# Optimization experiments

Measured on AMD Instinct MI355X. Metric: run time of the kernel, lower is better.

Reference implementation:

```python
import jax, jax.numpy as jnp
import numpy as np

GAMMA = 0.9
SCALE_BASE = 512.0


def _xpos(x, downscale=False):
    """XPOS rotary embedding (torchscale variant) applied to x: (B, L, D)."""
    B, L, D = x.shape
    half = D // 2
    # per-channel magnitude base: ((2i) + 0.4*D) / (1.4*D), i over even channels
    scale_vec = (jnp.arange(0, D, 2, dtype=jnp.float32) + 0.4 * D) / (1.4 * D)  # (half,)
    power = jnp.arange(L, dtype=jnp.float32) / SCALE_BASE                        # (L,)
    scale = scale_vec[None, :] ** power[:, None]                                 # (L, half)
    if downscale:
        scale = 1.0 / scale
    # fixed sinusoidal frequencies over `half` dims
    inv_freq = 1.0 / (10000.0 ** (jnp.arange(half, dtype=jnp.float32) / half))   # (half,)
    sinusoid = jnp.arange(L, dtype=jnp.float32)[:, None] * inv_freq[None, :]     # (L, half)
    sin = jnp.repeat(jnp.sin(sinusoid) * scale, 2, axis=-1)                      # (L, D) interleaved dup
    cos = jnp.repeat(jnp.cos(sinusoid) * scale, 2, axis=-1)
    # rotate_every_two: (x0,x1,x2,x3,...) -> (-x1,x0,-x3,x2,...)
    x_even = x[..., 0::2]
    x_odd = x[..., 1::2]
    rot = jnp.stack((-x_odd, x_even), axis=-1).reshape(x.shape)
    return x * cos + rot * sin


def _get_D(seq_len):
    n = jnp.arange(seq_len, dtype=jnp.float32)[:, None]
    m = jnp.arange(seq_len, dtype=jnp.float32)[None, :]
    D = GAMMA ** jnp.abs(n - m)  # non-causal decay, no NaNs since gamma > 0
    return D


def setup_inputs() -> dict:
    key = jax.random.key(0)
    k1, k2, k3, k4 = jax.random.split(key, 4)
    B, L, H, Dh = 8, 2048, 1024, 1024
    X = jax.random.normal(k1, (B, L, H), dtype=jnp.float32)
    W_Q = jax.random.normal(k2, (H, Dh), dtype=jnp.float32) / H
    W_K = jax.random.normal(k3, (H, Dh), dtype=jnp.float32) / H
    W_V = jax.random.normal(k4, (H, Dh), dtype=jnp.float32) / H
    return {"X": X, "W_Q": W_Q, "W_K": W_K, "W_V": W_V}


def reference(X, W_Q, W_K, W_V):
    B, L, H = X.shape
    D = _get_D(L)                       # (L, L)
    Q = _xpos(X @ W_Q)                  # (B, L, Dh)
    K = _xpos(X @ W_K, downscale=True)  # (B, L, Dh)
    V = X @ W_V                         # (B, L, Dv)
    scores = jnp.einsum('bqd,bkd->bqk', Q, K)   # (B, L, L)
    p_attn = jax.nn.softmax(scores, axis=-1)
    p_attn = p_attn * D[None, :, :]              # elementwise decay AFTER softmax
    return jnp.einsum('bqk,bkv->bqv', p_attn, V)
```

## Files before the change

kernel.cpp:

```cpp
#include <hip/hip_runtime.h>
#include <math.h>


#define LDIM 2048
#define HDIM 1024
#define MTOT 16384

typedef unsigned short u16;
typedef unsigned int u32;
typedef __attribute__((ext_vector_type(4))) float f32x4;
typedef __attribute__((ext_vector_type(8))) short s16x8;

#define GLD16(gp, lp) __builtin_amdgcn_global_load_lds( \
    (const __attribute__((address_space(1))) void*)(gp), \
    (__attribute__((address_space(3))) void*)(lp), 16, 0, 0)

__device__ __forceinline__ u16 f2bf(float f) {
    unsigned u = __float_as_uint(f);
    return (u16)((u + 0x7FFFu + ((u >> 16) & 1u)) >> 16);
}

__device__ __forceinline__ void sincos_rev(float ang, float* sn, float* cs) {
    double dr = (double)ang * 0.15915494309189535;
    dr -= __builtin_floor(dr);
    float fr = (float)dr;
    float s_, c_;
    asm("v_sin_f32 %0, %1" : "=v"(s_) : "v"(fr));
    asm("v_cos_f32 %0, %1" : "=v"(c_) : "v"(fr));
    *sn = s_; *cs = c_;
}

__device__ __forceinline__ void gemm256q(const u16* __restrict__ A,
                                         const u16* __restrict__ B,
                                         int lda, int ldb, int K, int m0, int n0,
                                         char* smem, int tid, f32x4 (*acc)[4])
{
    const int wv = tid >> 6, ln = tid & 63;
    const int wm = wv >> 2, wn = wv & 3;
    const int lr = ln & 15, lg = ln >> 4;
    const int srow = tid >> 3;
    const int scol = ((tid & 7) ^ (srow & 7)) * 8;

    const u16* ap[4];
    const u16* bp[4];
#pragma unroll
    for (int r = 0; r < 4; ++r) {
        ap[r] = A + (size_t)(m0 + r * 64 + srow) * lda + scol;
        bp[r] = B + (size_t)(n0 + r * 64 + srow) * ldb + scol;
    }

    int arow[8], brow[4];
#pragma unroll
    for (int fm = 0; fm < 8; ++fm) arow[fm] = (wm * 128 + fm * 16 + lr) * 128;
#pragma unroll
    for (int fn = 0; fn < 4; ++fn) brow[fn] = 32768 + (wn * 64 + fn * 16 + lr) * 128;
    int slotb[2];
#pragma unroll
    for (int kk = 0; kk < 2; ++kk) slotb[kk] = (((kk << 2) | lg) ^ (lr & 7)) << 4;

#define SGA0(e_) do{ char* d_=smem+(e_)*65536+tid*16;       GLD16(ap[0],d_); GLD16(ap[1],d_+8192); ap[0]+=64; ap[1]+=64; }while(0)
#define SGA1(e_) do{ char* d_=smem+(e_)*65536+16384+tid*16; GLD16(ap[2],d_); GLD16(ap[3],d_+8192); ap[2]+=64; ap[3]+=64; }while(0)
#define SGB0(e_) do{ char* d_=smem+(e_)*65536+32768+tid*16; GLD16(bp[0],d_); GLD16(bp[1],d_+8192); bp[0]+=64; bp[1]+=64; }while(0)
#define SGB1(e_) do{ char* d_=smem+(e_)*65536+49152+tid*16; GLD16(bp[2],d_); GLD16(bp[3],d_+8192); bp[2]+=64; bp[3]+=64; }while(0)

#define RD_A(Bb_, mh) do {                                                    \
        _Pragma("unroll") for (int fm_ = 0; fm_ < 4; ++fm_)                   \
            _Pragma("unroll") for (int kk_ = 0; kk_ < 2; ++kk_)               \
                aq[fm_ * 2 + kk_] = *(const s16x8*)((Bb_) +                   \
                    arow[(mh) * 4 + fm_] + slotb[kk_]);                       \
    } while (0)
#define RD_B(Bb_, nh, dst) do {                                               \
        _Pragma("unroll") for (int fn_ = 0; fn_ < 2; ++fn_)                   \
            _Pragma("unroll") for (int kk_ = 0; kk_ < 2; ++kk_)               \
                dst[fn_ * 2 + kk_] = *(const s16x8*)((Bb_) +                  \
                    brow[(nh) * 2 + fn_] + slotb[kk_]);                       \
    } while (0)

#define MFMA16(mh, nh, bq_) do { __builtin_amdgcn_s_setprio(1);               \
        _Pragma("unroll") for (int fm_ = 0; fm_ < 4; ++fm_)                   \
            _Pragma("unroll") for (int fn_ = 0; fn_ < 2; ++fn_)               \
                _Pragma("unroll") for (int kk_ = 0; kk_ < 2; ++kk_)           \
                    acc[(mh) * 4 + fm_][(nh) * 2 + fn_] =                     \
                        __builtin_amdgcn_mfma_f32_16x16x32_bf16(              \
                            aq[fm_ * 2 + kk_], bq_[fn_ * 2 + kk_],            \
                            acc[(mh) * 4 + fm_][(nh) * 2 + fn_], 0, 0, 0);    \
        __builtin_amdgcn_s_setprio(0); } while (0)

#define BAR do { __builtin_amdgcn_sched_barrier(0);                           \
                 __builtin_amdgcn_s_barrier();                                \
                 __builtin_amdgcn_sched_barrier(0); } while (0)

    const int nk = K >> 6;

    SGA0(0); SGB0(0); SGA1(0); SGB1(0);

    s16x8 aq[8], b0[4], b1[4];

#pragma unroll 1
    for (int t = 0; t < nk; ++t) {
        const int d = t & 1, e = d ^ 1;
        const bool pre = (t + 1 < nk);
        const char* Bb = smem + d * 65536;

        if (pre) { SGA0(e); SGB0(e);
                   asm volatile("s_waitcnt vmcnt(4)" ::: "memory"); }
        else     { asm volatile("s_waitcnt vmcnt(0)" ::: "memory"); }
        BAR;
        RD_A(Bb, 0); RD_B(Bb, 0, b0); if (pre) SGA1(e);
        BAR; MFMA16(0, 0, b0); BAR;
        RD_B(Bb, 1, b1); if (pre) SGB1(e);
        BAR; MFMA16(0, 1, b1); BAR;
        RD_A(Bb, 1);
        BAR; MFMA16(1, 1, b1); BAR;
        BAR; MFMA16(1, 0, b0); BAR;
    }
    __syncthreads();
#undef SGA0
#undef SGA1
#undef SGB0
#undef SGB1
#undef RD_A
#undef RD_B
#undef MFMA16
#undef BAR
}

__global__ __launch_bounds__(256) void prep_all(
    const float* __restrict__ X,
    const float* __restrict__ Wq, const float* __restrict__ Wk,
    const float* __restrict__ Wv,
    u16* __restrict__ Xb, u16* __restrict__ WT,
    u32* __restrict__ CSq, u32* __restrict__ CSk)
{
    __shared__ float L[64][65];
    const int bid = blockIdx.x;
    if (bid < 2048) {
        const int n4 = MTOT * HDIM / 4;
        int i = bid * 256 + threadIdx.x;
        const int stride = 2048 * 256;
        for (; i < n4; i += stride) {
            float4 v = ((const float4*)X)[i];
            ushort4 o = make_ushort4(f2bf(v.x), f2bf(v.y), f2bf(v.z), f2bf(v.w));
            ((ushort4*)Xb)[i] = o;
        }
    } else if (bid < 4096) {
        const int l = bid - 2048;
        for (int ih = threadIdx.x; ih < 512; ih += 256) {
            float invf = exp2f(-13.287712379549449f * (1.f / 512.f) * (float)ih);
            float sn, cs;
            sincos_rev((float)l * invf, &sn, &cs);
            float l2sv = log2f(((float)(2 * ih) + 409.6f) * (1.f / 1433.6f));
            float e = (float)l * (1.f / 512.f) * l2sv;
            float sq = exp2f(e), sk = exp2f(-e);
            CSq[l * 512 + ih] = (u32)f2bf(cs * sq) | ((u32)f2bf(sn * sq) << 16);
            CSk[l * 512 + ih] = (u32)f2bf(cs * sk) | ((u32)f2bf(sn * sk) << 16);
        }
    } else {
        const int r = bid - 4096;
        const int z = r >> 8;
        const int y = (r >> 4) & 15;
        const int x = r & 15;
        const float* Wz = (z == 0) ? Wq : (z == 1) ? Wk : Wv;
        u16* Oz = WT + (size_t)z * HDIM * HDIM;
        const int k0 = y * 64, n0 = x * 64;
        const int t = threadIdx.x;
        const int r_ = t >> 4, c4 = (t & 15) * 4;
#pragma unroll
        for (int it = 0; it < 4; ++it) {
            const int row = it * 16 + r_;
            float4 v = *(const float4*)&Wz[(size_t)(k0 + row) * HDIM + n0 + c4];
            L[row][c4 + 0] = v.x; L[row][c4 + 1] = v.y;
            L[row][c4 + 2] = v.z; L[row][c4 + 3] = v.w;
        }
        __syncthreads();
#pragma unroll
        for (int it = 0; it < 4; ++it) {
            const int orow = it * 16 + r_;
            ushort4 o = make_ushort4(f2bf(L[c4 + 0][orow]), f2bf(L[c4 + 1][orow]),
                                     f2bf(L[c4 + 2][orow]), f2bf(L[c4 + 3][orow]));
            *(ushort4*)&Oz[(size_t)(n0 + orow) * HDIM + k0 + c4] = o;
        }
    }
}

__global__ __launch_bounds__(512, 2) void qkv_gemm(
    const u16* __restrict__ Xb, const u16* __restrict__ WT,
    const u32* __restrict__ CSq, const u32* __restrict__ CSk,
    u16* __restrict__ Qb, u16* __restrict__ Kb, u16* __restrict__ Vt)
{
    __shared__ __align__(16) char smem[256 * 264 * 2];
    const int bid = blockIdx.x;
    const int xcd = bid & 7, t = bid >> 3;
    const int m8 = t & 7;
    const int n_ = (t >> 3) & 3;
    const int z  = t >> 5;
    const int m0 = (xcd * 8 + m8) * 256;
    const int n0 = n_ * 256;
    const int tid = threadIdx.x;

    f32x4 acc[8][4] = {};

    gemm256q(Xb, WT + (size_t)z * HDIM * HDIM, HDIM, HDIM, HDIM, m0, n0, smem, tid, acc);

    const int wv = tid >> 6, ln = tid & 63;
    const int wm = wv >> 2, wn = wv & 3;
    const int lr = ln & 15, lg = ln >> 4;
    const int l0 = m0 & (LDIM - 1);
    u16* T = (u16*)smem;

    if (z < 2) {
        const u32* CS = (z == 0) ? CSq : CSk;
#pragma unroll
        for (int fn = 0; fn < 4; ++fn) {
            const int gc = n0 + wn * 64 + fn * 16 + lr;
            const int ih = gc >> 1;
            const float sgn = (gc & 1) ? 1.f : -1.f;
            const u32* tb = CS + (size_t)l0 * 512 + ih;
#pragma unroll
            for (int fm = 0; fm < 8; ++fm) {
#pragma unroll
                for (int reg = 0; reg < 4; ++reg) {
                    const int rowl = wm * 128 + fm * 16 + lg * 4 + reg;
                    u32 v = tb[(size_t)rowl * 512];
                    float cs = __uint_as_float(v << 16);
                    float sn = __uint_as_float(v & 0xFFFF0000u);
                    float c = acc[fm][fn][reg];
                    float p = __shfl_xor(c, 1);
                    T[rowl * 264 + wn * 64 + fn * 16 + lr] =
                        f2bf(c * cs + sgn * p * sn);
                }
            }
        }
        __syncthreads();
        u16* Out = (z == 0) ? Qb : Kb;
        const int row_ = tid >> 5, slot = tid & 31;
#pragma unroll
        for (int g = 0; g < 16; ++g) {
            const int row = g * 16 + row_;
            s16x8 v = *(const s16x8*)&T[row * 264 + slot * 8];
            *(s16x8*)&Out[(size_t)(m0 + row) * HDIM + n0 + slot * 8] = v;
        }
    } else {
#pragma unroll
        for (int fn = 0; fn < 4; ++fn)
#pragma unroll
            for (int fm = 0; fm < 8; ++fm) {
                ushort4 o = make_ushort4(f2bf(acc[fm][fn][0]), f2bf(acc[fm][fn][1]),
                                         f2bf(acc[fm][fn][2]), f2bf(acc[fm][fn][3]));
                *(ushort4*)&T[(wn * 64 + fn * 16 + lr) * 264 +
                              wm * 128 + fm * 16 + lg * 4] = o;
            }
        __syncthreads();
        const int b = m0 >> 11;
        const int row_ = tid >> 5, slot = tid & 31;
#pragma unroll
        for (int g = 0; g < 16; ++g) {
            const int row = g * 16 + row_;
            s16x8 v = *(const s16x8*)&T[row * 264 + slot * 8];
            *(s16x8*)&Vt[((size_t)b * HDIM + n0 + row) * LDIM + l0 + slot * 8] = v;
        }
    }
}

__global__ __launch_bounds__(512, 2) void qk_gemm(
    const u16* __restrict__ Q, const u16* __restrict__ Km,
    u16* __restrict__ Wm, float* __restrict__ Zp)
{
    __shared__ __align__(16) char smem[256 * 264 * 2];
    __shared__ float Zl[4][256];
    const int bid = blockIdx.x;
    const int b = bid & 7, t = bid >> 3;
    const int mt = t & 7;
    const int nt = t >> 3;
    const int m0 = mt * 256;
    const int n0 = nt * 256;
    const int tid = threadIdx.x;

    f32x4 acc[8][4] = {};

    gemm256q(Q + (size_t)b * LDIM * HDIM, Km + (size_t)b * LDIM * HDIM,
             HDIM, HDIM, HDIM, m0, n0, smem, tid, acc);

    const int wv = tid >> 6, ln = tid & 63;
    const int wm = wv >> 2, wn = wv & 3;
    const int lr = ln & 15, lg = ln >> 4;
    u16* T = (u16*)smem;
    const float LOG2E = 1.4426950408889634f;
    const float LOG2G = -0.15200309344504997f;

#pragma unroll
    for (int fm = 0; fm < 8; ++fm) {
        float ps[4] = {0.f, 0.f, 0.f, 0.f};
#pragma unroll
        for (int fn = 0; fn < 4; ++fn) {
            const int gk = n0 + wn * 64 + fn * 16 + lr;
#pragma unroll
            for (int reg = 0; reg < 4; ++reg) {
                const int mloc = wm * 128 + fm * 16 + lg * 4 + reg;
                const int gq = m0 + mloc;
                float t1 = acc[fm][fn][reg] * LOG2E;
                float e = exp2f(t1);
                int dd = gq - gk; dd = dd < 0 ? -dd : dd;
                ps[reg] += e;
                T[mloc * 264 + wn * 64 + fn * 16 + lr] =
                    f2bf(exp2f(t1 + (float)dd * LOG2G));
            }
        }
#pragma unroll
        for (int reg = 0; reg < 4; ++reg) {
            float s = ps[reg];
            s += __shfl_xor(s, 1); s += __shfl_xor(s, 2);
            s += __shfl_xor(s, 4); s += __shfl_xor(s, 8);
            if (lr == 0)
                Zl[wn][wm * 128 + fm * 16 + lg * 4 + reg] = s;
        }
    }
    __syncthreads();

    const int row_ = tid >> 5, slot = tid & 31;
#pragma unroll
    for (int g = 0; g < 16; ++g) {
        const int row = g * 16 + row_;
        s16x8 v = *(const s16x8*)&T[row * 264 + slot * 8];
        *(s16x8*)&Wm[((size_t)b * LDIM + m0 + row) * LDIM + n0 + slot * 8] = v;
    }
    if (tid < 256)
        Zp[((size_t)b * 8 + nt) * LDIM + m0 + tid] =
            Zl[0][tid] + Zl[1][tid] + Zl[2][tid] + Zl[3][tid];
}

__global__ __launch_bounds__(512, 2) void pv_gemm(
    const u16* __restrict__ Wm, const u16* __restrict__ Vt,
    const float* __restrict__ Zp, float* __restrict__ Out)
{
    __shared__ __align__(16) char smem[2 * 65536];
    __shared__ float Zinv[256];
    const int bid = blockIdx.x;
    const int b = bid & 7, t = bid >> 3;
    const int mt4 = t & 3;
    const int nt = (t >> 2) & 3;
    const int mtH = t >> 4;
    const int m0 = (mtH * 4 + mt4) * 256;
    const int n0 = nt * 256;
    const int tid = threadIdx.x;

    if (tid < 256) {
        float zz = 0.f;
#pragma unroll
        for (int nb = 0; nb < 8; ++nb)
            zz += Zp[((size_t)b * 8 + nb) * LDIM + m0 + tid];
        Zinv[tid] = 1.0f / zz;
    }
    __syncthreads();

    f32x4 acc[8][4] = {};

    gemm256q(Wm + (size_t)b * LDIM * LDIM, Vt + (size_t)b * HDIM * LDIM,
             LDIM, LDIM, LDIM, m0, n0, smem, tid, acc);

    const int wv = tid >> 6, ln = tid & 63;
    const int wm = wv >> 2, wn = wv & 3;
    const int lr = ln & 15, lg = ln >> 4;
    float* Ob = Out + (size_t)b * LDIM * HDIM;
#pragma unroll
    for (int fm = 0; fm < 8; ++fm)
#pragma unroll
        for (int fn = 0; fn < 4; ++fn) {
            const int gn = n0 + wn * 64 + fn * 16 + lr;
#pragma unroll
            for (int reg = 0; reg < 4; ++reg) {
                const int row = wm * 128 + fm * 16 + lg * 4 + reg;
                Ob[(size_t)(m0 + row) * HDIM + gn] = acc[fm][fn][reg] * Zinv[row];
            }
        }
}

extern "C" void kernel_launch(void* const* d_in, const int* in_sizes, int n_in,
                              void* d_out, int out_size, void* d_ws, size_t ws_size,
                              hipStream_t stream)
{
    (void)in_sizes; (void)n_in; (void)out_size; (void)ws_size;
    const float* X  = (const float*)d_in[0];
    const float* Wq = (const float*)d_in[1];
    const float* Wk = (const float*)d_in[2];
    const float* Wv = (const float*)d_in[3];
    char* ws = (char*)d_ws;
    const size_t MB = 1024 * 1024;

    u16* Wmat = (u16*)ws;
    u16* Xb   = (u16*)ws;
    u16* WT   = (u16*)(ws + 32 * MB);
    u16* Qb   = (u16*)(ws + 64 * MB);
    u16* Kb   = (u16*)(ws + 96 * MB);
    u16* Vt   = (u16*)(ws + 128 * MB);
    float* Zp = (float*)(ws + 160 * MB);
    u32* CSq  = (u32*)(ws + 161 * MB);
    u32* CSk  = (u32*)(ws + 165 * MB);

    prep_all<<<4864, 256, 0, stream>>>(X, Wq, Wk, Wv, Xb, WT, CSq, CSk);
    qkv_gemm<<<768, 512, 0, stream>>>(Xb, WT, CSq, CSk, Qb, Kb, Vt);
    qk_gemm<<<512, 512, 0, stream>>>(Qb, Kb, Wmat, Zp);
    pv_gemm<<<256, 512, 0, stream>>>(Wmat, Vt, Zp, (float*)d_out);
}
```

Baseline: 309.5 us.

## Simplify shared GEMM main loop to whole-tile prefetch with one barrier per step

```diff
diff --git a/kernel.cpp b/kernel.cpp
--- a/kernel.cpp
+++ b/kernel.cpp
@@ -30,7 +30,7 @@
     *sn = s_; *cs = c_;
 }
 
-__device__ __forceinline__ void gemm256q(const u16* __restrict__ A,
+__device__ __forceinline__ void gemm256h(const u16* __restrict__ A,
                                          const u16* __restrict__ B,
                                          int lda, int ldb, int K, int m0, int n0,
                                          char* smem, int tid, f32x4 (*acc)[4])
@@ -58,10 +58,12 @@
 #pragma unroll
     for (int kk = 0; kk < 2; ++kk) slotb[kk] = (((kk << 2) | lg) ^ (lr & 7)) << 4;
 
-#define SGA0(e_) do{ char* d_=smem+(e_)*65536+tid*16;       GLD16(ap[0],d_); GLD16(ap[1],d_+8192); ap[0]+=64; ap[1]+=64; }while(0)
-#define SGA1(e_) do{ char* d_=smem+(e_)*65536+16384+tid*16; GLD16(ap[2],d_); GLD16(ap[3],d_+8192); ap[2]+=64; ap[3]+=64; }while(0)
-#define SGB0(e_) do{ char* d_=smem+(e_)*65536+32768+tid*16; GLD16(bp[0],d_); GLD16(bp[1],d_+8192); bp[0]+=64; bp[1]+=64; }while(0)
-#define SGB1(e_) do{ char* d_=smem+(e_)*65536+49152+tid*16; GLD16(bp[2],d_); GLD16(bp[3],d_+8192); bp[2]+=64; bp[3]+=64; }while(0)
+#define STAGEALL(e_) do { char* d_ = smem + (e_) * 65536 + tid * 16;          \
+        _Pragma("unroll") for (int r_ = 0; r_ < 4; ++r_) {                    \
+            GLD16(ap[r_], d_ + r_ * 8192);          ap[r_] += 64; }           \
+        _Pragma("unroll") for (int r_ = 0; r_ < 4; ++r_) {                    \
+            GLD16(bp[r_], d_ + 32768 + r_ * 8192);  bp[r_] += 64; }           \
+    } while (0)
 
 #define RD_A(Bb_, mh) do {                                                    \
         _Pragma("unroll") for (int fm_ = 0; fm_ < 4; ++fm_)                   \
@@ -76,7 +78,7 @@
                     brow[(nh) * 2 + fn_] + slotb[kk_]);                       \
     } while (0)
 
-#define MFMA16(mh, nh, bq_) do { __builtin_amdgcn_s_setprio(1);               \
+#define MFMA16(mh, nh, bq_) do {                                              \
         _Pragma("unroll") for (int fm_ = 0; fm_ < 4; ++fm_)                   \
             _Pragma("unroll") for (int fn_ = 0; fn_ < 2; ++fn_)               \
                 _Pragma("unroll") for (int kk_ = 0; kk_ < 2; ++kk_)           \
@@ -84,45 +86,34 @@
                         __builtin_amdgcn_mfma_f32_16x16x32_bf16(              \
                             aq[fm_ * 2 + kk_], bq_[fn_ * 2 + kk_],            \
                             acc[(mh) * 4 + fm_][(nh) * 2 + fn_], 0, 0, 0);    \
-        __builtin_amdgcn_s_setprio(0); } while (0)
-
-#define BAR do { __builtin_amdgcn_sched_barrier(0);                           \
-                 __builtin_amdgcn_s_barrier();                                \
-                 __builtin_amdgcn_sched_barrier(0); } while (0)
+    } while (0)
 
     const int nk = K >> 6;
 
-    SGA0(0); SGB0(0); SGA1(0); SGB1(0);
+    STAGEALL(0);
+    __syncthreads();
 
     s16x8 aq[8], b0[4], b1[4];
 
 #pragma unroll 1
     for (int t = 0; t < nk; ++t) {
         const int d = t & 1, e = d ^ 1;
-        const bool pre = (t + 1 < nk);
+        if (t + 1 < nk) STAGEALL(e);
         const char* Bb = smem + d * 65536;
-
-        if (pre) { SGA0(e); SGB0(e);
-                   asm volatile("s_waitcnt vmcnt(4)" ::: "memory"); }
-        else     { asm volatile("s_waitcnt vmcnt(0)" ::: "memory"); }
-        BAR;
-        RD_A(Bb, 0); RD_B(Bb, 0, b0); if (pre) SGA1(e);
-        BAR; MFMA16(0, 0, b0); BAR;
-        RD_B(Bb, 1, b1); if (pre) SGB1(e);
-        BAR; MFMA16(0, 1, b1); BAR;
+        RD_A(Bb, 0); RD_B(Bb, 0, b0);
+        MFMA16(0, 0, b0);
+        RD_B(Bb, 1, b1);
+        MFMA16(0, 1, b1);
         RD_A(Bb, 1);
-        BAR; MFMA16(1, 1, b1); BAR;
-        BAR; MFMA16(1, 0, b0); BAR;
+        MFMA16(1, 1, b1);
+        MFMA16(1, 0, b0);
+        __syncthreads();
     }
     __syncthreads();
-#undef SGA0
-#undef SGA1
-#undef SGB0
-#undef SGB1
+#undef STAGEALL
 #undef RD_A
 #undef RD_B
 #undef MFMA16
-#undef BAR
 }
 
 __global__ __launch_bounds__(256) void prep_all(
@@ -200,7 +191,7 @@
 
     f32x4 acc[8][4] = {};
 
-    gemm256q(Xb, WT + (size_t)z * HDIM * HDIM, HDIM, HDIM, HDIM, m0, n0, smem, tid, acc);
+    gemm256h(Xb, WT + (size_t)z * HDIM * HDIM, HDIM, HDIM, HDIM, m0, n0, smem, tid, acc);
 
     const int wv = tid >> 6, ln = tid & 63;
     const int wm = wv >> 2, wn = wv & 3;
@@ -278,7 +269,7 @@
 
     f32x4 acc[8][4] = {};
 
-    gemm256q(Q + (size_t)b * LDIM * HDIM, Km + (size_t)b * LDIM * HDIM,
+    gemm256h(Q + (size_t)b * LDIM * HDIM, Km + (size_t)b * LDIM * HDIM,
              HDIM, HDIM, HDIM, m0, n0, smem, tid, acc);
 
     const int wv = tid >> 6, ln = tid & 63;
@@ -355,7 +346,7 @@
 
     f32x4 acc[8][4] = {};
 
-    gemm256q(Wm + (size_t)b * LDIM * LDIM, Vt + (size_t)b * HDIM * LDIM,
+    gemm256h(Wm + (size_t)b * LDIM * LDIM, Vt + (size_t)b * HDIM * LDIM,
              LDIM, LDIM, LDIM, m0, n0, smem, tid, acc);
 
     const int wv = tid >> 6, ln = tid & 63;
```

Result: faster. 289.5 us (median of 2 runs) (-6.5%).
